# Optimization experiments

Measured on AMD Instinct MI355X. Metric: run time of the kernel, lower is better.

## Reference

```python
import jax, jax.numpy as jnp
import numpy as np

K = 3                # k_const
NUM_CLASSES = 10
CLASS_SIZE = 5000
NUM_TRAIN = NUM_CLASSES * CLASS_SIZE   # 50000
DIGIT_WIDTH = 256
NUM_TEST = 4096


def setup_inputs() -> dict:
    key = jax.random.key(0)
    k1, k2 = jax.random.split(key)
    training_set = jax.random.randint(k1, (NUM_TRAIN, DIGIT_WIDTH), 0, 2, dtype=jnp.int32)
    test_set = jax.random.randint(k2, (NUM_TEST, DIGIT_WIDTH), 0, 2, dtype=jnp.int32)
    return {"training_set": training_set, "test_set": test_set}


def reference(training_set, test_set):
    # Hamming distance between binary vectors a,b: sum(a XOR b)
    # = sum(a) + sum(b) - 2*dot(a,b); computed as one int matmul instead of
    # materializing the [T, N, D] XOR tensor.
    tr_sum = jnp.sum(training_set, axis=1)                    # [N]
    te_sum = jnp.sum(test_set, axis=1)                        # [T]
    inner = jnp.matmul(test_set, training_set.T)              # [T, N] int32
    dists = te_sum[:, None] + tr_sum[None, :] - 2 * inner     # [T, N]

    # Original loop keeps the K smallest distances, ties won by the earlier
    # training index (strict '<' insertion). lax.top_k on negated distances
    # breaks ties by smaller index, matching that behavior.
    _, knn_idx = jax.lax.top_k(-dists, K)                     # [T, K]
    labels = knn_idx // CLASS_SIZE                            # [T, K]

    # Majority vote per test sample; argmax returns first max on ties,
    # same as torch.argmax in the original.
    T = test_set.shape[0]
    votes = jnp.zeros((T, NUM_CLASSES), dtype=jnp.int32)
    votes = votes.at[jnp.arange(T)[:, None], labels].add(1)   # [T, C]
    return jnp.argmax(votes, axis=1)                          # [T]
```

## Files before the change

kernel.cpp:

```cpp
#include <hip/hip_runtime.h>
#include <stdint.h>

typedef unsigned long long u64;
typedef unsigned int u32;
typedef int v4i  __attribute__((ext_vector_type(4)));
typedef int v16i __attribute__((ext_vector_type(16)));

#define NUM_TRAIN   50000
#define NUM_TEST    4096
#define CLASS_SIZE  5000
#define TRAIN_PAD   50176
#define TOT_TILES   1568

#define SZ_TRAIN   ((size_t)TRAIN_PAD * 256)
#define SZ_TEST    ((size_t)NUM_TEST * 256)
#define SZ_TESUM   ((size_t)NUM_TEST * 4)
#define OFF_TEST   (SZ_TRAIN)
#define OFF_TESUM  (OFF_TEST + SZ_TEST)
#define OFF_PART   (OFF_TESUM + SZ_TESUM)
#define WS_NEED(NCH) (OFF_PART + (size_t)NUM_TEST * (NCH) * 3 * 4)

__device__ __forceinline__ void insert3(u32& k0, u32& k1, u32& k2, u32 key) {
    u32 m1, m2;
    asm("v_med3_u32 %0, %1, %2, %3" : "=v"(m1) : "v"(k0), "v"(k1), "v"(key));
    asm("v_med3_u32 %0, %1, %2, %3" : "=v"(m2) : "v"(k1), "v"(k2), "v"(key));
    k0 = min(k0, key);
    k1 = m1; k2 = m2;
}
__device__ __forceinline__ void merge3(u32& a0, u32& a1, u32& a2,
                                       u32 b0, u32 b1, u32 b2) {
    u32 hi0 = max(a0, b0);
    u32 lo1 = min(a1, b1);
    u32 c0  = min(a0, b0);
    u32 c1  = min(hi0, lo1);
    u32 c2  = min(max(lo1, hi0), min(a2, b2));
    a0 = c0; a1 = c1; a2 = c2;
}
__device__ __forceinline__ int wave_sum(int s) {
    #pragma unroll
    for (int off = 1; off < 64; off <<= 1) s += __shfl_xor(s, off);
    return s;
}

__global__ __launch_bounds__(256) void pack_all(const int* __restrict__ train,
                                                const int* __restrict__ test,
                                                char* __restrict__ dstA,
                                                char* __restrict__ dstB,
                                                int* __restrict__ tesum) {
    int r    = (blockIdx.x * 256 + threadIdx.x) >> 6;
    int lane = threadIdx.x & 63;
    if (r < TRAIN_PAD) {
        int4 v = make_int4(0, 0, 0, 0);
        if (r < NUM_TRAIN)
            v = *reinterpret_cast<const int4*>(train + (size_t)r * 256 + lane * 4);
        u32 w = (u32)(v.x & 1) | ((u32)(v.y & 1) << 8)
              | ((u32)(v.z & 1) << 16) | ((u32)(v.w & 1) << 24);
        *reinterpret_cast<u32*>(dstA + (size_t)r * 256 + lane * 4) = w;
    } else {
        int rt = r - TRAIN_PAD;
        int4 v = *reinterpret_cast<const int4*>(test + (size_t)rt * 256 + lane * 4);
        u32 w = (u32)((1 - 2 * v.x) & 0xFF) | ((u32)((1 - 2 * v.y) & 0xFF) << 8)
              | ((u32)((1 - 2 * v.z) & 0xFF) << 16) | ((u32)((1 - 2 * v.w) & 0xFF) << 24);
        *reinterpret_cast<u32*>(dstB + (size_t)rt * 256 + lane * 4) = w;
        int total = wave_sum(v.x + v.y + v.z + v.w);
        if (lane == 0) tesum[rt] = total;
    }
}

template<int NCH>
__global__ __launch_bounds__(256) void mfma_knn(const char* __restrict__ A,
                                                const char* __restrict__ Bt,
                                                const int* __restrict__ tesum,
                                                u32* __restrict__ partial) {
    constexpr int TILES  = TOT_TILES / NCH;
    constexpr int CHROWS = TRAIN_PAD / NCH;
    static_assert((TILES & 1) == 0, "2-phase dbuf loop needs even TILES");
    const int cg   = blockIdx.x / NCH;
    const int c    = blockIdx.x % NCH;
    const int tid  = threadIdx.x;
    const int wid  = tid >> 6;
    const int lane = tid & 63;
    const int a    = lane & 31;
    const int kh   = lane >> 5;

    const int col0 = cg * 256 + wid * 64 + a;
    const int col1 = col0 + 32;
    v4i bf0[8], bf1[8];
    {
        const char* bp0 = Bt + (size_t)col0 * 256 + kh * 16;
        const char* bp1 = Bt + (size_t)col1 * 256 + kh * 16;
        #pragma unroll
        for (int kk = 0; kk < 8; ++kk) {
            bf0[kk] = *reinterpret_cast<const v4i*>(bp0 + kk * 32);
            bf1[kk] = *reinterpret_cast<const v4i*>(bp1 + kk * 32);
        }
    }
    const u32 base0 = ((u32)tesum[col0] << 16);
    const u32 base1 = ((u32)tesum[col1] << 16);

    __shared__ char lds[2][8192];
    char* rd[8];
    #pragma unroll
    for (int kk = 0; kk < 8; ++kk)
        rd[kk] = &lds[0][kk * 1024 + kh * 512 + ((a ^ kk) & 31) * 16];

    const int grow = tid >> 3, gc = tid & 7;
    const char* gsrc0 = A + (size_t)c * CHROWS * 256 + grow * 256 + gc * 32;
    char* w0 = &lds[0][gc * 1024 +       ((grow ^ gc) & 31) * 16];
    char* w1 = &lds[0][gc * 1024 + 512 + ((grow ^ gc) & 31) * 16];

    u32 p00 = 0x7FFFFFFFu, p01 = 0x7FFFFFFFu, p02 = 0x7FFFFFFFu;
    u32 p10 = 0x7FFFFFFFu, p11 = 0x7FFFFFFFu, p12 = 0x7FFFFFFFu;

    {
        uint4 s0 = *reinterpret_cast<const uint4*>(gsrc0);
        uint4 s1 = *reinterpret_cast<const uint4*>(gsrc0 + 16);
        *reinterpret_cast<uint4*>(w0) = s0;
        *reinterpret_cast<uint4*>(w1) = s1;
    }
    __syncthreads();

#define TILE_STEP(TT, RB, WB)                                                 \
    {                                                                         \
        const int tt = (TT);                                                  \
        uint4 s0, s1;                                                         \
        const bool pf = (tt + 1 < TILES);                                     \
        if (pf) {                                                             \
            const char* g = gsrc0 + (size_t)(tt + 1) * 8192;                  \
            s0 = *reinterpret_cast<const uint4*>(g);                          \
            s1 = *reinterpret_cast<const uint4*>(g + 16);                     \
        }                                                                     \
        v16i acc0 = {0,0,0,0,0,0,0,0,0,0,0,0,0,0,0,0};                        \
        v16i acc1 = {0,0,0,0,0,0,0,0,0,0,0,0,0,0,0,0};                        \
        __builtin_amdgcn_s_setprio(1);                                        \
        _Pragma("unroll")                                                     \
        for (int kk = 0; kk < 8; ++kk) {                                      \
            v4i af = *reinterpret_cast<const v4i*>(rd[kk] + (RB) * 8192);     \
            acc0 = __builtin_amdgcn_mfma_i32_32x32x32_i8(af, bf0[kk], acc0, 0, 0, 0); \
            acc1 = __builtin_amdgcn_mfma_i32_32x32x32_i8(af, bf1[kk], acc1, 0, 0, 0); \
        }                                                                     \
        __builtin_amdgcn_s_setprio(0);                                        \
        const int tbase = c * CHROWS + tt * 32;                               \
        const u32 kb0 = base0 + (u32)(tbase + 4 * kh);                        \
        const u32 kb1 = base1 + (u32)(tbase + 4 * kh);                        \
        if (tbase + 32 <= NUM_TRAIN) {                                        \
            _Pragma("unroll")                                                 \
            for (int g = 0; g < 16; ++g) {                                    \
                const int row = (g & 3) + 8 * (g >> 2);                       \
                insert3(p00, p01, p02, ((u32)acc0[g] << 16) + kb0 + (u32)row);\
                insert3(p10, p11, p12, ((u32)acc1[g] << 16) + kb1 + (u32)row);\
            }                                                                 \
        } else {                                                              \
            _Pragma("unroll")                                                 \
            for (int g = 0; g < 16; ++g) {                                    \
                const int row = (g & 3) + 8 * (g >> 2);                       \
                const int idx = tbase + 4 * kh + row;                         \
                u32 key0 = (idx < NUM_TRAIN)                                  \
                    ? (((u32)acc0[g] << 16) + kb0 + (u32)row) : 0xFFFFFFFFu;  \
                u32 key1 = (idx < NUM_TRAIN)                                  \
                    ? (((u32)acc1[g] << 16) + kb1 + (u32)row) : 0xFFFFFFFFu;  \
                insert3(p00, p01, p02, key0);                                 \
                insert3(p10, p11, p12, key1);                                 \
            }                                                                 \
        }                                                                     \
        if (pf) {                                                             \
            *reinterpret_cast<uint4*>(w0 + (WB) * 8192) = s0;                 \
            *reinterpret_cast<uint4*>(w1 + (WB) * 8192) = s1;                 \
        }                                                                     \
        __syncthreads();                                                      \
    }

    #pragma unroll 1
    for (int t = 0; t < TILES; t += 2) {
        TILE_STEP(t,     0, 1);
        TILE_STEP(t + 1, 1, 0);
    }
#undef TILE_STEP

    u32 o0, o1, o2;
    o0 = __shfl_xor(p00, 32); o1 = __shfl_xor(p01, 32); o2 = __shfl_xor(p02, 32);
    merge3(p00, p01, p02, o0, o1, o2);
    o0 = __shfl_xor(p10, 32); o1 = __shfl_xor(p11, 32); o2 = __shfl_xor(p12, 32);
    merge3(p10, p11, p12, o0, o1, o2);
    if (kh == 0) {
        u32* d0 = partial + ((size_t)c * NUM_TEST + col0) * 3;
        d0[0] = p00; d0[1] = p01; d0[2] = p02;
        u32* d1 = partial + ((size_t)c * NUM_TEST + col1) * 3;
        d1[0] = p10; d1[1] = p11; d1[2] = p12;
    }
}

template<int NCH>
__global__ __launch_bounds__(256) void vote_knn(const u32* __restrict__ partial,
                                                int* __restrict__ out) {
    int t = blockIdx.x * 256 + threadIdx.x;
    if (t >= NUM_TEST) return;
    const u32* p0 = partial + (size_t)t * 3;
    u32 a0 = p0[0], a1 = p0[1], a2 = p0[2];
    #pragma unroll 8
    for (int c = 1; c < NCH; ++c) {
        const u32* q = partial + ((size_t)c * NUM_TEST + t) * 3;
        merge3(a0, a1, a2, q[0], q[1], q[2]);
    }
    const int l0 = (int)(a0 & 0xFFFFu) / CLASS_SIZE;
    const int l1 = (int)(a1 & 0xFFFFu) / CLASS_SIZE;
    const int l2 = (int)(a2 & 0xFFFFu) / CLASS_SIZE;
    int winner;
    if (l0 == l1 || l0 == l2)      winner = l0;
    else if (l1 == l2)             winner = l1;
    else winner = min(l0, min(l1, l2));
    out[t] = winner;
}

#define TT          8
#define NCHUNK      4
#define CHUNK_ROWS  (NUM_TRAIN / NCHUNK)

__device__ __forceinline__ void insert3_minmax(u32& k0, u32& k1, u32& k2, u32 key) {
    u32 m0 = min(k0, key);
    u32 m1 = min(k1, max(k0, key));
    u32 m2 = min(k2, max(k1, key));
    k0 = m0; k1 = m1; k2 = m2;
}

__global__ void pack_kernel(const int* __restrict__ train,
                            const int* __restrict__ test,
                            u64* __restrict__ packed) {
    int wave = (blockIdx.x * blockDim.x + threadIdx.x) >> 6;
    int lane = threadIdx.x & 63;
    const int* src = (wave < NUM_TRAIN)
                       ? (train + (size_t)wave * 256)
                       : (test + (size_t)(wave - NUM_TRAIN) * 256);
    int4 v = *reinterpret_cast<const int4*>(src + lane * 4);
    u64 b0 = __ballot(v.x & 1);
    u64 b1 = __ballot(v.y & 1);
    u64 b2 = __ballot(v.z & 1);
    u64 b3 = __ballot(v.w & 1);
    if (lane == 0) {
        u64* dst = packed + (size_t)wave * 4;
        dst[0] = b0; dst[1] = b1; dst[2] = b2; dst[3] = b3;
    }
}

__global__ __launch_bounds__(256) void knn_kernel(const u32* __restrict__ packed,
                                                  u32* __restrict__ partial) {
    const int g    = blockIdx.x >> 2;
    const int c    = blockIdx.x & 3;
    const int tid  = threadIdx.x;
    const int base = g * TT;
    const uint4* rows  = (const uint4*)packed;
    const u32*  testp  = packed + (size_t)NUM_TRAIN * 8;

    u32 te[TT][8];
    #pragma unroll
    for (int s = 0; s < TT; ++s) {
        const u32* p = testp + (size_t)(base + s) * 8;
        #pragma unroll
        for (int j = 0; j < 8; ++j) te[s][j] = p[j];
    }
    u32 k0[TT], k1[TT], k2[TT];
    #pragma unroll
    for (int s = 0; s < TT; ++s) { k0[s] = k1[s] = k2[s] = 0x7FFFFFFFu; }

    const int start = c * CHUNK_ROWS;
    const int end   = start + CHUNK_ROWS;
    for (int r = start + tid; r < end; r += 256) {
        uint4 a0 = rows[(size_t)r * 2];
        uint4 a1 = rows[(size_t)r * 2 + 1];
        #pragma unroll
        for (int s = 0; s < TT; ++s) {
            int d = __popc(a0.x ^ te[s][0]);
            d += __popc(a0.y ^ te[s][1]);
            d += __popc(a0.z ^ te[s][2]);
            d += __popc(a0.w ^ te[s][3]);
            d += __popc(a1.x ^ te[s][4]);
            d += __popc(a1.y ^ te[s][5]);
            d += __popc(a1.z ^ te[s][6]);
            d += __popc(a1.w ^ te[s][7]);
            u32 key = ((u32)d << 16) | (u32)r;
            insert3_minmax(k0[s], k1[s], k2[s], key);
        }
    }
    #pragma unroll
    for (int s = 0; s < TT; ++s) {
        for (int off = 1; off < 64; off <<= 1) {
            u32 o0 = __shfl_xor(k0[s], off);
            u32 o1 = __shfl_xor(k1[s], off);
            u32 o2 = __shfl_xor(k2[s], off);
            merge3(k0[s], k1[s], k2[s], o0, o1, o2);
        }
    }
    __shared__ u32 red[4][TT][3];
    const int wave = tid >> 6, lane = tid & 63;
    if (lane == 0) {
        #pragma unroll
        for (int s = 0; s < TT; ++s) {
            red[wave][s][0] = k0[s];
            red[wave][s][1] = k1[s];
            red[wave][s][2] = k2[s];
        }
    }
    __syncthreads();
    if (tid < TT) {
        const int s = tid;
        u32 a0 = red[0][s][0], a1 = red[0][s][1], a2 = red[0][s][2];
        #pragma unroll
        for (int w = 1; w < 4; ++w)
            merge3(a0, a1, a2, red[w][s][0], red[w][s][1], red[w][s][2]);
        u32* dst = partial + ((size_t)(base + s) * NCHUNK + c) * 3;
        dst[0] = a0; dst[1] = a1; dst[2] = a2;
    }
}

__global__ __launch_bounds__(256) void merge_kernel(const u32* __restrict__ partial,
                                                    int* __restrict__ out) {
    int t = blockIdx.x * blockDim.x + threadIdx.x;
    if (t >= NUM_TEST) return;
    const u32* p = partial + (size_t)t * NCHUNK * 3;
    u32 a0 = p[0], a1 = p[1], a2 = p[2];
    #pragma unroll
    for (int c = 1; c < NCHUNK; ++c)
        merge3(a0, a1, a2, p[c * 3 + 0], p[c * 3 + 1], p[c * 3 + 2]);
    const int l0 = (int)(a0 & 0xFFFFu) / CLASS_SIZE;
    const int l1 = (int)(a1 & 0xFFFFu) / CLASS_SIZE;
    const int l2 = (int)(a2 & 0xFFFFu) / CLASS_SIZE;
    int winner;
    if (l0 == l1 || l0 == l2)      winner = l0;
    else if (l1 == l2)             winner = l1;
    else winner = min(l0, min(l1, l2));
    out[t] = winner;
}

extern "C" void kernel_launch(void* const* d_in, const int* in_sizes, int n_in,
                              void* d_out, int out_size, void* d_ws, size_t ws_size,
                              hipStream_t stream) {
    const int* train = (const int*)d_in[0];
    const int* test  = (const int*)d_in[1];
    int* out = (int*)d_out;

    if (ws_size >= WS_NEED(112)) {
        char* train_i8 = (char*)d_ws;
        char* test_i8  = (char*)d_ws + OFF_TEST;
        int*  tesum    = (int*)((char*)d_ws + OFF_TESUM);
        u32*  partial  = (u32*)((char*)d_ws + OFF_PART);

        pack_all<<<(TRAIN_PAD + NUM_TEST) / 4, 256, 0, stream>>>(train, test,
                                                                 train_i8, test_i8, tesum);
        mfma_knn<112><<<16 * 112, 256, 0, stream>>>(train_i8, test_i8, tesum, partial);
        vote_knn<112><<<NUM_TEST / 256, 256, 0, stream>>>(partial, out);
    } else {
        u64* packed = (u64*)d_ws;
        u32* partial = (u32*)((char*)d_ws + (size_t)(NUM_TRAIN + NUM_TEST) * 4 * sizeof(u64));
        const int total_rows = NUM_TRAIN + NUM_TEST;
        pack_kernel<<<total_rows / 4, 256, 0, stream>>>(train, test, packed);
        knn_kernel<<<(NUM_TEST / TT) * NCHUNK, 256, 0, stream>>>((const u32*)packed, partial);
        merge_kernel<<<(NUM_TEST + 255) / 256, 256, 0, stream>>>(partial, out);
    }
}
```

Before: 91.48 us.

## Pre-swizzle train tiles in pack kernel and stream them via direct global-to-LDS loads

```diff
diff --git a/kernel.cpp b/kernel.cpp
--- a/kernel.cpp
+++ b/kernel.cpp
@@ -40,6 +40,11 @@
     #pragma unroll
     for (int off = 1; off < 64; off <<= 1) s += __shfl_xor(s, off);
     return s;
+}
+__device__ __forceinline__ void gload16(const void* g, void* l) {
+    __builtin_amdgcn_global_load_lds(
+        (const __attribute__((address_space(1))) unsigned int*)g,
+        (__attribute__((address_space(3))) unsigned int*)l, 16, 0, 0);
 }
 
 __global__ __launch_bounds__(256) void pack_all(const int* __restrict__ train,
@@ -55,7 +60,13 @@
             v = *reinterpret_cast<const int4*>(train + (size_t)r * 256 + lane * 4);
         u32 w = (u32)(v.x & 1) | ((u32)(v.y & 1) << 8)
               | ((u32)(v.z & 1) << 16) | ((u32)(v.w & 1) << 24);
-        *reinterpret_cast<u32*>(dstA + (size_t)r * 256 + lane * 4) = w;
+        const int tile = r >> 5, row = r & 31;
+        const int kk   = lane >> 3;
+        const int kh   = (lane >> 2) & 1;
+        const int slot = (row ^ kk) & 31;
+        size_t dst = (size_t)tile * 8192 + kk * 1024 + kh * 512
+                   + (size_t)slot * 16 + (lane & 3) * 4;
+        *reinterpret_cast<u32*>(dstA + dst) = w;
     } else {
         int rt = r - TRAIN_PAD;
         int4 v = *reinterpret_cast<const int4*>(test + (size_t)rt * 256 + lane * 4);
@@ -75,6 +86,7 @@
     constexpr int TILES  = TOT_TILES / NCH;
     constexpr int CHROWS = TRAIN_PAD / NCH;
     static_assert((TILES & 1) == 0, "2-phase dbuf loop needs even TILES");
+    static_assert((CHROWS & 31) == 0, "chunk must be whole tiles");
     const int cg   = blockIdx.x / NCH;
     const int c    = blockIdx.x % NCH;
     const int tid  = threadIdx.x;
@@ -104,31 +116,23 @@
     for (int kk = 0; kk < 8; ++kk)
         rd[kk] = &lds[0][kk * 1024 + kh * 512 + ((a ^ kk) & 31) * 16];
 
-    const int grow = tid >> 3, gc = tid & 7;
-    const char* gsrc0 = A + (size_t)c * CHROWS * 256 + grow * 256 + gc * 32;
-    char* w0 = &lds[0][gc * 1024 +       ((grow ^ gc) & 31) * 16];
-    char* w1 = &lds[0][gc * 1024 + 512 + ((grow ^ gc) & 31) * 16];
+    const char* asrc = A + (size_t)(c * (CHROWS / 32)) * 8192
+                         + wid * 2048 + lane * 16;
 
     u32 p00 = 0x7FFFFFFFu, p01 = 0x7FFFFFFFu, p02 = 0x7FFFFFFFu;
     u32 p10 = 0x7FFFFFFFu, p11 = 0x7FFFFFFFu, p12 = 0x7FFFFFFFu;
 
-    {
-        uint4 s0 = *reinterpret_cast<const uint4*>(gsrc0);
-        uint4 s1 = *reinterpret_cast<const uint4*>(gsrc0 + 16);
-        *reinterpret_cast<uint4*>(w0) = s0;
-        *reinterpret_cast<uint4*>(w1) = s1;
-    }
+    gload16(asrc,        &lds[0][wid * 2048]);
+    gload16(asrc + 1024, &lds[0][wid * 2048 + 1024]);
     __syncthreads();
 
 #define TILE_STEP(TT, RB, WB)                                                 \
     {                                                                         \
         const int tt = (TT);                                                  \
-        uint4 s0, s1;                                                         \
-        const bool pf = (tt + 1 < TILES);                                     \
-        if (pf) {                                                             \
-            const char* g = gsrc0 + (size_t)(tt + 1) * 8192;                  \
-            s0 = *reinterpret_cast<const uint4*>(g);                          \
-            s1 = *reinterpret_cast<const uint4*>(g + 16);                     \
+        if (tt + 1 < TILES) {                                                 \
+            const char* g = asrc + (size_t)(tt + 1) * 8192;                   \
+            gload16(g,        &lds[WB][wid * 2048]);                          \
+            gload16(g + 1024, &lds[WB][wid * 2048 + 1024]);                   \
         }                                                                     \
         v16i acc0 = {0,0,0,0,0,0,0,0,0,0,0,0,0,0,0,0};                        \
         v16i acc1 = {0,0,0,0,0,0,0,0,0,0,0,0,0,0,0,0};                        \
@@ -163,10 +167,6 @@
                 insert3(p10, p11, p12, key1);                                 \
             }                                                                 \
         }                                                                     \
-        if (pf) {                                                             \
-            *reinterpret_cast<uint4*>(w0 + (WB) * 8192) = s0;                 \
-            *reinterpret_cast<uint4*>(w1 + (WB) * 8192) = s1;                 \
-        }                                                                     \
         __syncthreads();                                                      \
     }
 
@@ -339,14 +339,14 @@
     int* out = (int*)d_out;
 
     if (ws_size >= WS_NEED(112)) {
-        char* train_i8 = (char*)d_ws;
-        char* test_i8  = (char*)d_ws + OFF_TEST;
-        int*  tesum    = (int*)((char*)d_ws + OFF_TESUM);
-        u32*  partial  = (u32*)((char*)d_ws + OFF_PART);
+        char* train_swz = (char*)d_ws;
+        char* test_i8   = (char*)d_ws + OFF_TEST;
+        int*  tesum     = (int*)((char*)d_ws + OFF_TESUM);
+        u32*  partial   = (u32*)((char*)d_ws + OFF_PART);
 
         pack_all<<<(TRAIN_PAD + NUM_TEST) / 4, 256, 0, stream>>>(train, test,
-                                                                 train_i8, test_i8, tesum);
-        mfma_knn<112><<<16 * 112, 256, 0, stream>>>(train_i8, test_i8, tesum, partial);
+                                                                 train_swz, test_i8, tesum);
+        mfma_knn<112><<<16 * 112, 256, 0, stream>>>(train_swz, test_i8, tesum, partial);
         vote_knn<112><<<NUM_TEST / 256, 256, 0, stream>>>(partial, out);
     } else {
         u64* packed = (u64*)d_ws;
```

Result: no change. 92.79 us (+1.4%).

## Split MFMA accumulation chains and replace serial top-3 insert with sorting-network reduce

Applied to the files above, without the earlier changes.

```diff
diff --git a/kernel.cpp b/kernel.cpp
--- a/kernel.cpp
+++ b/kernel.cpp
@@ -20,13 +20,6 @@
 #define OFF_PART   (OFF_TESUM + SZ_TESUM)
 #define WS_NEED(NCH) (OFF_PART + (size_t)NUM_TEST * (NCH) * 3 * 4)
 
-__device__ __forceinline__ void insert3(u32& k0, u32& k1, u32& k2, u32 key) {
-    u32 m1, m2;
-    asm("v_med3_u32 %0, %1, %2, %3" : "=v"(m1) : "v"(k0), "v"(k1), "v"(key));
-    asm("v_med3_u32 %0, %1, %2, %3" : "=v"(m2) : "v"(k1), "v"(k2), "v"(key));
-    k0 = min(k0, key);
-    k1 = m1; k2 = m2;
-}
 __device__ __forceinline__ void merge3(u32& a0, u32& a1, u32& a2,
                                        u32 b0, u32 b1, u32 b2) {
     u32 hi0 = max(a0, b0);
@@ -40,6 +33,37 @@
     #pragma unroll
     for (int off = 1; off < 64; off <<= 1) s += __shfl_xor(s, off);
     return s;
+}
+
+template<bool GUARD>
+__device__ __forceinline__ void reduce16(const v16i& A, u32 kb, int idxb,
+                                         u32& p0, u32& p1, u32& p2) {
+    u32 lo[8], hi[8];
+    #pragma unroll
+    for (int i = 0; i < 8; ++i) {
+        const int g0 = 2 * i, g1 = 2 * i + 1;
+        const int r0 = (g0 & 3) + 8 * (g0 >> 2);
+        const int r1 = (g1 & 3) + 8 * (g1 >> 2);
+        u32 ka = ((u32)A[g0] << 16) + kb + (u32)r0;
+        u32 kc = ((u32)A[g1] << 16) + kb + (u32)r1;
+        if (GUARD) {
+            if (idxb + r0 >= NUM_TRAIN) ka = 0xFFFFFFFFu;
+            if (idxb + r1 >= NUM_TRAIN) kc = 0xFFFFFFFFu;
+        }
+        lo[i] = min(ka, kc); hi[i] = max(ka, kc);
+    }
+    u32 t0[4], t1[4], t2[4];
+    #pragma unroll
+    for (int j = 0; j < 4; ++j) {
+        u32 la = lo[2 * j], lb = lo[2 * j + 1];
+        u32 ha = hi[2 * j], hb = hi[2 * j + 1];
+        u32 m = max(la, lb), n = min(ha, hb);
+        t0[j] = min(la, lb); t1[j] = min(m, n); t2[j] = max(m, n);
+    }
+    merge3(t0[0], t1[0], t2[0], t0[1], t1[1], t2[1]);
+    merge3(t0[2], t1[2], t2[2], t0[3], t1[3], t2[3]);
+    merge3(t0[0], t1[0], t2[0], t0[2], t1[2], t2[2]);
+    merge3(p0, p1, p2, t0[0], t1[0], t2[0]);
 }
 
 __global__ __launch_bounds__(256) void pack_all(const int* __restrict__ train,
@@ -130,38 +154,33 @@
             s0 = *reinterpret_cast<const uint4*>(g);                          \
             s1 = *reinterpret_cast<const uint4*>(g + 16);                     \
         }                                                                     \
-        v16i acc0 = {0,0,0,0,0,0,0,0,0,0,0,0,0,0,0,0};                        \
-        v16i acc1 = {0,0,0,0,0,0,0,0,0,0,0,0,0,0,0,0};                        \
+        v16i a0e = {0,0,0,0,0,0,0,0,0,0,0,0,0,0,0,0};                         \
+        v16i a0o = {0,0,0,0,0,0,0,0,0,0,0,0,0,0,0,0};                         \
+        v16i a1e = {0,0,0,0,0,0,0,0,0,0,0,0,0,0,0,0};                         \
+        v16i a1o = {0,0,0,0,0,0,0,0,0,0,0,0,0,0,0,0};                         \
         __builtin_amdgcn_s_setprio(1);                                        \
         _Pragma("unroll")                                                     \
-        for (int kk = 0; kk < 8; ++kk) {                                      \
-            v4i af = *reinterpret_cast<const v4i*>(rd[kk] + (RB) * 8192);     \
-            acc0 = __builtin_amdgcn_mfma_i32_32x32x32_i8(af, bf0[kk], acc0, 0, 0, 0); \
-            acc1 = __builtin_amdgcn_mfma_i32_32x32x32_i8(af, bf1[kk], acc1, 0, 0, 0); \
+        for (int kk = 0; kk < 8; kk += 2) {                                   \
+            v4i afe = *reinterpret_cast<const v4i*>(rd[kk]     + (RB) * 8192);\
+            v4i afo = *reinterpret_cast<const v4i*>(rd[kk + 1] + (RB) * 8192);\
+            a0e = __builtin_amdgcn_mfma_i32_32x32x32_i8(afe, bf0[kk],     a0e, 0, 0, 0); \
+            a1e = __builtin_amdgcn_mfma_i32_32x32x32_i8(afe, bf1[kk],     a1e, 0, 0, 0); \
+            a0o = __builtin_amdgcn_mfma_i32_32x32x32_i8(afo, bf0[kk + 1], a0o, 0, 0, 0); \
+            a1o = __builtin_amdgcn_mfma_i32_32x32x32_i8(afo, bf1[kk + 1], a1o, 0, 0, 0); \
         }                                                                     \
         __builtin_amdgcn_s_setprio(0);                                        \
+        v16i A0 = a0e + a0o;                                                  \
+        v16i A1 = a1e + a1o;                                                  \
         const int tbase = c * CHROWS + tt * 32;                               \
         const u32 kb0 = base0 + (u32)(tbase + 4 * kh);                        \
         const u32 kb1 = base1 + (u32)(tbase + 4 * kh);                        \
+        const int idxb = tbase + 4 * kh;                                      \
         if (tbase + 32 <= NUM_TRAIN) {                                        \
-            _Pragma("unroll")                                                 \
-            for (int g = 0; g < 16; ++g) {                                    \
-                const int row = (g & 3) + 8 * (g >> 2);                       \
-                insert3(p00, p01, p02, ((u32)acc0[g] << 16) + kb0 + (u32)row);\
-                insert3(p10, p11, p12, ((u32)acc1[g] << 16) + kb1 + (u32)row);\
-            }                                                                 \
+            reduce16<false>(A0, kb0, idxb, p00, p01, p02);                    \
+            reduce16<false>(A1, kb1, idxb, p10, p11, p12);                    \
         } else {                                                              \
-            _Pragma("unroll")                                                 \
-            for (int g = 0; g < 16; ++g) {                                    \
-                const int row = (g & 3) + 8 * (g >> 2);                       \
-                const int idx = tbase + 4 * kh + row;                         \
-                u32 key0 = (idx < NUM_TRAIN)                                  \
-                    ? (((u32)acc0[g] << 16) + kb0 + (u32)row) : 0xFFFFFFFFu;  \
-                u32 key1 = (idx < NUM_TRAIN)                                  \
-                    ? (((u32)acc1[g] << 16) + kb1 + (u32)row) : 0xFFFFFFFFu;  \
-                insert3(p00, p01, p02, key0);                                 \
-                insert3(p10, p11, p12, key1);                                 \
-            }                                                                 \
+            reduce16<true>(A0, kb0, idxb, p00, p01, p02);                     \
+            reduce16<true>(A1, kb1, idxb, p10, p11, p12);                     \
         }                                                                     \
         if (pf) {                                                             \
             *reinterpret_cast<uint4*>(w0 + (WB) * 8192) = s0;                 \
```

Result: slower. 98.51 us (+7.7%).
